# Performance work log

Measured on AMD Instinct MI355X. Metric: run time of the kernel, lower is better.

The kernel has to match this reference:

```python
import jax, jax.numpy as jnp
import numpy as np

N_ROWS = 4_000_000
M_LFS = 20
EPS = 1e-06


def setup_inputs() -> dict:
    key = jax.random.key(0)
    k1, k2, k3 = jax.random.split(key, 3)
    # labeling matrix with entries in {-1, 0, 1}
    L = jax.random.randint(k1, (N_ROWS, M_LFS), 0, 3, dtype=jnp.int32) - 1
    # unconstrained alpha param (sigmoid applied in forward), beta probabilities
    alpha = jax.random.normal(k2, (M_LFS,), dtype=jnp.float32)
    beta = jax.random.uniform(k3, (M_LFS,), dtype=jnp.float32, minval=0.3, maxval=0.5)
    return {"L": L, "alpha": alpha, "beta": beta}


def reference(L, alpha, beta):
    # alpha is clamped to [0,1] via sigmoid (clamp_params)
    a = jax.nn.sigmoid(alpha)  # [m]
    abstain = (1.0 - beta)                      # factor when lambda_j == 0
    agree = beta * a                            # factor when lambda_j == y
    disagree = beta * (1.0 - a)                 # factor when lambda_j == -y
    # per-row, per-LF factors for y=+1 and y=-1  -> [n, m]
    f_pos = jnp.where(L == 0, abstain, jnp.where(L == 1, agree, disagree))
    f_neg = jnp.where(L == 0, abstain, jnp.where(L == 1, disagree, agree))
    mu = jnp.prod(f_pos, axis=-1) + jnp.prod(f_neg, axis=-1)  # [n]
    nll = -jnp.sum(jnp.log(mu + EPS))
    return nll
```

## Files before the change

kernel.cpp:

```cpp
#include <hip/hip_runtime.h>
#include <math.h>

#define M_LFS 20
#define EPS 1e-6f
#define BLOCK 256
#define GRID 2048

__global__ __launch_bounds__(BLOCK) void ratner_nll_kernel(
    const int* __restrict__ L,
    const float* __restrict__ alpha,
    const float* __restrict__ beta,
    float* __restrict__ out,
    int n_rows)
{
    __shared__ float s_ab[M_LFS];
    __shared__ float s_ag[M_LFS];
    __shared__ float s_di[M_LFS];

    const int tid = threadIdx.x;
    if (tid < M_LFS) {
        float al = alpha[tid];
        float b  = beta[tid];
        float a  = 1.0f / (1.0f + __expf(-al));
        s_ab[tid] = 1.0f - b;
        s_ag[tid] = b * a;
        s_di[tid] = b * (1.0f - a);
    }
    __syncthreads();

    float local = 0.0f;

    const int gid    = blockIdx.x * BLOCK + tid;
    const int stride = gridDim.x * BLOCK;

    for (int row = gid; row < n_rows; row += stride) {
        const int4* rp = (const int4*)(L + (size_t)row * M_LFS);
        float pp = 1.0f;
        float pn = 1.0f;
#pragma unroll
        for (int c = 0; c < 5; ++c) {
            int4 v = rp[c];
            int ls0 = v.x, ls1 = v.y, ls2 = v.z, ls3 = v.w;
#pragma unroll
            for (int k = 0; k < 4; ++k) {
                int j = c * 4 + k;
                int l = (k == 0) ? ls0 : (k == 1) ? ls1 : (k == 2) ? ls2 : ls3;
                float ab = s_ab[j];
                float ag = s_ag[j];
                float di = s_di[j];
                float fp = (l == 0) ? ab : ((l == 1) ? ag : di);
                float fn = (l == 0) ? ab : ((l == 1) ? di : ag);
                pp *= fp;
                pn *= fn;
            }
        }
        float mu = pp + pn;
        local += __logf(mu + EPS);
    }

#pragma unroll
    for (int off = 32; off > 0; off >>= 1)
        local += __shfl_down(local, off, 64);

    __shared__ float s_wave[BLOCK / 64];
    const int wave = tid >> 6;
    if ((tid & 63) == 0) s_wave[wave] = local;
    __syncthreads();

    if (tid == 0) {
        float bsum = 0.0f;
#pragma unroll
        for (int w = 0; w < BLOCK / 64; ++w) bsum += s_wave[w];
        atomicAdd(out, -bsum);
    }
}

extern "C" void kernel_launch(void* const* d_in, const int* in_sizes, int n_in,
                              void* d_out, int out_size, void* d_ws, size_t ws_size,
                              hipStream_t stream) {
    const int*   L     = (const int*)d_in[0];
    const float* alpha = (const float*)d_in[1];
    const float* beta  = (const float*)d_in[2];
    float*       out   = (float*)d_out;

    const int n_rows = in_sizes[0] / M_LFS;

    hipMemsetAsync(out, 0, sizeof(float), stream);

    ratner_nll_kernel<<<GRID, BLOCK, 0, stream>>>(L, alpha, beta, out, n_rows);
}
```

Baseline: 478.2 us.

## Stage row tiles through LDS with coalesced int4 loads per wave

Each wave now loads a contiguous 64-row chunk of L using fully coalesced int4 loads across lanes, transposes it into padded LDS, and then each lane reads its row from LDS. The original layout had each thread read 80 strided bytes, which coalesces poorly. The LF constants are also hoisted into scalar registers via readfirstlane. The cost is extra LDS traffic and more register use. Synchronisation relies on inline s_waitcnt rather than a barrier, which is only intra-wave safe and depends on compiler ordering.

Result: faster. 441.5 us (-7.7%).

```diff
diff --git a/kernel.cpp b/kernel.cpp
--- a/kernel.cpp
+++ b/kernel.cpp
@@ -5,6 +5,8 @@
 #define EPS 1e-6f
 #define BLOCK 256
 #define GRID 2048
+#define WPB (BLOCK / 64)
+#define ROW_PAD 21
 
 __global__ __launch_bounds__(BLOCK) void ratner_nll_kernel(
     const int* __restrict__ L,
@@ -13,65 +15,82 @@
     float* __restrict__ out,
     int n_rows)
 {
-    __shared__ float s_ab[M_LFS];
-    __shared__ float s_ag[M_LFS];
-    __shared__ float s_di[M_LFS];
+    __shared__ float s_ab[M_LFS], s_ag[M_LFS], s_di[M_LFS];
+    __shared__ int   s_tile[WPB][64 * ROW_PAD];
+    __shared__ float s_wred[WPB];
 
-    const int tid = threadIdx.x;
+    const int tid  = threadIdx.x;
+    const int lane = tid & 63;
+    const int wave = tid >> 6;
+
     if (tid < M_LFS) {
-        float al = alpha[tid];
-        float b  = beta[tid];
-        float a  = 1.0f / (1.0f + __expf(-al));
+        float a = 1.0f / (1.0f + __expf(-alpha[tid]));
+        float b = beta[tid];
         s_ab[tid] = 1.0f - b;
         s_ag[tid] = b * a;
         s_di[tid] = b * (1.0f - a);
     }
     __syncthreads();
 
+    float r_ab[M_LFS], r_ag[M_LFS], r_di[M_LFS];
+#pragma unroll
+    for (int j = 0; j < M_LFS; ++j) {
+        r_ab[j] = __int_as_float(__builtin_amdgcn_readfirstlane(__float_as_int(s_ab[j])));
+        r_ag[j] = __int_as_float(__builtin_amdgcn_readfirstlane(__float_as_int(s_ag[j])));
+        r_di[j] = __int_as_float(__builtin_amdgcn_readfirstlane(__float_as_int(s_di[j])));
+    }
+
+    int* tile = &s_tile[wave][0];
+    const int4* gp = (const int4*)L;
+    const long  n_i4 = (long)n_rows * 5;
+
     float local = 0.0f;
 
-    const int gid    = blockIdx.x * BLOCK + tid;
-    const int stride = gridDim.x * BLOCK;
+    const int n_groups = (n_rows + 63) >> 6;
+    const int n_waves  = gridDim.x * WPB;
 
-    for (int row = gid; row < n_rows; row += stride) {
-        const int4* rp = (const int4*)(L + (size_t)row * M_LFS);
-        float pp = 1.0f;
-        float pn = 1.0f;
+    for (int grp = blockIdx.x * WPB + wave; grp < n_groups; grp += n_waves) {
+        const long base = (long)grp * 320;
+
 #pragma unroll
-        for (int c = 0; c < 5; ++c) {
-            int4 v = rp[c];
-            int ls0 = v.x, ls1 = v.y, ls2 = v.z, ls3 = v.w;
+        for (int k = 0; k < 5; ++k) {
+            const int  q = lane + (k << 6);
+            const long g = base + q;
+            int4 v = make_int4(0, 0, 0, 0);
+            if (g < n_i4) v = gp[g];
+            int* dst = tile + (q / 5) * ROW_PAD + (q % 5) * 4;
+            dst[0] = v.x; dst[1] = v.y; dst[2] = v.z; dst[3] = v.w;
+        }
+        __asm__ __volatile__("s_waitcnt lgkmcnt(0)" ::: "memory");
+
+        const int row = (grp << 6) + lane;
+        if (row < n_rows) {
+            const int* rp = tile + lane * ROW_PAD;
+            float pp = 1.0f, pn = 1.0f;
 #pragma unroll
-            for (int k = 0; k < 4; ++k) {
-                int j = c * 4 + k;
-                int l = (k == 0) ? ls0 : (k == 1) ? ls1 : (k == 2) ? ls2 : ls3;
-                float ab = s_ab[j];
-                float ag = s_ag[j];
-                float di = s_di[j];
-                float fp = (l == 0) ? ab : ((l == 1) ? ag : di);
-                float fn = (l == 0) ? ab : ((l == 1) ? di : ag);
+            for (int j = 0; j < M_LFS; ++j) {
+                const int   l  = rp[j];
+                const float ab = r_ab[j];
+                const float fp = (l == 0) ? ab : ((l == 1) ? r_ag[j] : r_di[j]);
+                const float fn = (l == 0) ? ab : ((l == 1) ? r_di[j] : r_ag[j]);
                 pp *= fp;
                 pn *= fn;
             }
+            local += __logf(pp + pn + EPS);
         }
-        float mu = pp + pn;
-        local += __logf(mu + EPS);
+        __asm__ __volatile__("s_waitcnt lgkmcnt(0)" ::: "memory");
     }
 
 #pragma unroll
     for (int off = 32; off > 0; off >>= 1)
         local += __shfl_down(local, off, 64);
-
-    __shared__ float s_wave[BLOCK / 64];
-    const int wave = tid >> 6;
-    if ((tid & 63) == 0) s_wave[wave] = local;
+    if (lane == 0) s_wred[wave] = local;
     __syncthreads();
-
     if (tid == 0) {
-        float bsum = 0.0f;
+        float b = 0.0f;
 #pragma unroll
-        for (int w = 0; w < BLOCK / 64; ++w) bsum += s_wave[w];
-        atomicAdd(out, -bsum);
+        for (int w = 0; w < WPB; ++w) b += s_wred[w];
+        atomicAdd(out, -b);
     }
 }
 
```
